# Kernel optimization log

Hardware: AMD Instinct MI355X
Metric: run time of the kernel (lower is better)

Reference implementation:

```python
import jax, jax.numpy as jnp
import numpy as np

B, C, H, W = 1, 256, 48, 64
HW = H * W
HIDDEN, CTX = 128, 64
LEVELS, RADIUS = 4, 4
WIN = 2 * RADIUS + 1
P = WIN * WIN                     # 81 lookup points per level
CORR_DIM = P * LEVELS             # 324
TOP_K = 3
ITERS = 4
STEP_ROT, STEP_TRANS = 0.02, 0.02


def _sample_templates():
    # 12 directions x 3 scales + identity = 37 pose perturbations (as in __init__)
    base = [([0,0,0],[1,0,0]),([0,0,0],[-1,0,0]),([0,0,0],[0,1,0]),([0,0,0],[0,-1,0]),
            ([0,0,0],[0,0,1]),([0,0,0],[0,0,-1]),([1,0,0],[0,0,0]),([-1,0,0],[0,0,0]),
            ([0,1,0],[0,0,0]),([0,-1,0],[0,0,0]),([0,0,1],[0,0,0]),([0,0,-1],[0,0,0])]
    scales = np.array([0.25, 1.0, 4.0], np.float32)
    rot = np.repeat(np.array([r for r, _ in base], np.float32), 3, axis=0)
    trs = np.repeat(np.array([t for _, t in base], np.float32), 3, axis=0)
    sc = np.tile(scales, 12)
    axes = rot / np.clip(np.linalg.norm(rot, axis=1, keepdims=True), 1e-8, None)
    ha = STEP_ROT * sc / 2.0
    dq = np.stack([np.cos(ha), axes[:, 0]*np.sin(ha), axes[:, 1]*np.sin(ha), axes[:, 2]*np.sin(ha)], -1)
    dt = trs * (STEP_TRANS * sc[:, None])
    dq = np.concatenate([dq, [[1., 0., 0., 0.]]], 0)
    dt = np.concatenate([dt, [[0., 0., 0.]]], 0)
    return jnp.asarray(dq), jnp.asarray(dt)

DQ, DT = _sample_templates()     # (37,4), (37,3)
N_SAMPLES = DQ.shape[0]


def qmul(q, r):
    w1, x1, y1, z1 = jnp.moveaxis(q, -1, 0)
    w2, x2, y2, z2 = jnp.moveaxis(r, -1, 0)
    return jnp.stack([w1*w2 - x1*x2 - y1*y2 - z1*z2,
                      w1*x2 + x1*w2 + y1*z2 - z1*y2,
                      w1*y2 - x1*z2 + y1*w2 + z1*x2,
                      w1*z2 + x1*y2 - y1*x2 + z1*w2], -1)


def qapply(q, v):
    qv = jnp.concatenate([jnp.zeros(v.shape[:-1] + (1,), v.dtype), v], -1)
    qc = q * jnp.array([1., -1., -1., -1.], q.dtype)
    return qmul(qmul(q, qv), qc)[..., 1:]


def quat_to_R(q):
    w, x, y, z = jnp.moveaxis(q, -1, 0)
    R = jnp.stack([1-2*(y*y+z*z), 2*(x*y-w*z), 2*(x*z+w*y),
                   2*(x*y+w*z), 1-2*(x*x+z*z), 2*(y*z-w*x),
                   2*(x*z-w*y), 2*(y*z+w*x), 1-2*(x*x+y*y)], -1)
    return R.reshape(q.shape[:-1] + (3, 3))


def conv3(x, w, b):
    y = jax.lax.conv_general_dilated(x, w, (1, 1), 'SAME',
                                     dimension_numbers=('NCHW', 'OIHW', 'NCHW'))
    return y + b[None, :, None, None]


def bilinear_lookup(corr_flat, Hl, Wl, x, y):
    # corr_flat: (B,HW,Hl*Wl); x,y: (B,N,HW,P) -> (B,N,HW,P), zero padding outside
    x0 = jnp.floor(x)
    y0 = jnp.floor(y)
    out = jnp.zeros(x.shape, corr_flat.dtype)
    def gather(idx):
        g = lambda ix: jnp.take_along_axis(corr_flat, ix, axis=-1)
        return jax.vmap(g, in_axes=1, out_axes=1)(idx)   # vmap over N, no corr copy
    for dx_, dy_ in ((0, 0), (1, 0), (0, 1), (1, 1)):
        xi = x0 + dx_
        yi = y0 + dy_
        wgt = (1 - jnp.abs(x - xi)) * (1 - jnp.abs(y - yi))
        valid = (xi >= 0) & (xi < Wl) & (yi >= 0) & (yi < Hl)
        idx = (jnp.clip(yi, 0, Hl - 1) * Wl + jnp.clip(xi, 0, Wl - 1)).astype(jnp.int32)
        out = out + jnp.where(valid, wgt, 0.0) * gather(idx)
    return out


def _forward(fmap_rgb, fmap_depth, depth, context, intrinsics,
             Wz, bz, Wr, br, Wq, bq, Wh, bh, Wfc, bfc):
    f32 = jnp.float32
    fx = 60. + 40. * intrinsics[:, 0]
    fy = 60. + 40. * intrinsics[:, 1]
    cx = W / 2. + 4. * (intrinsics[:, 2] - 0.5)
    cy = H / 2. + 4. * (intrinsics[:, 3] - 0.5)
    d = 4.0 + 20.0 * depth                                  # (B,H,W) metric depth

    # 4D correlation pyramid: corr[b,i,:,:] = <fmap_depth pixel i, fmap_rgb>
    fd = fmap_depth.reshape(B, C, HW).transpose(0, 2, 1)    # (B,HW,C)
    corr = jnp.einsum('bic,bchw->bihw', fd, fmap_rgb) / jnp.sqrt(f32(C))
    pyramid = []
    cl, Hl, Wl = corr, H, W
    for _ in range(LEVELS):
        pyramid.append((cl.reshape(B, HW, Hl * Wl), Hl, Wl))
        cl = cl.reshape(B, HW, Hl // 2, 2, Wl // 2, 2).mean(axis=(3, 5))
        Hl //= 2
        Wl //= 2

    # back-projected depth points (B,HW,3)
    vv, uu = jnp.meshgrid(jnp.arange(H, dtype=f32), jnp.arange(W, dtype=f32), indexing='ij')
    uu = uu.reshape(HW)
    vv = vv.reshape(HW)
    df = d.reshape(B, HW)
    X = jnp.stack([(uu[None] - cx[:, None]) / fx[:, None] * df,
                   (vv[None] - cy[:, None]) / fy[:, None] * df, df], -1)

    off = jnp.arange(-RADIUS, RADIUS + 1, dtype=f32)
    oy, ox = jnp.meshgrid(off, off, indexing='ij')
    ox = ox.reshape(P)
    oy = oy.reshape(P)

    pose = jnp.tile(jnp.array([1., 0., 0., 0., 0., 0., 0.], f32)[None, :], (B, 1))
    h = jnp.zeros((B, HIDDEN, H, W), f32)

    for _ in range(ITERS):
        qc, tc = pose[:, :4], pose[:, 4:7]
        quats = qmul(qc[:, None, :], DQ[None])              # (B,N,4)
        quats = quats / jnp.linalg.norm(quats, axis=-1, keepdims=True)
        trans = tc[:, None, :] + qapply(qc[:, None, :], DT[None])
        Rm = quat_to_R(quats)                               # (B,N,3,3)
        Xc = jnp.einsum('bnij,bpj->bnpi', Rm, X) + trans[:, :, None, :]
        z = jnp.clip(Xc[..., 2], 0.1, None)
        u = fx[:, None, None] * Xc[..., 0] / z + cx[:, None, None]   # (B,N,HW)
        v = fy[:, None, None] * Xc[..., 1] / z + cy[:, None, None]
        feats = []
        for lvl, (cfl, Hl_, Wl_) in enumerate(pyramid):
            s = f32(2 ** lvl)
            xl = u[..., None] / s + ox
            yl = v[..., None] / s + oy
            feats.append(bilinear_lookup(cfl, Hl_, Wl_, xl, yl))
        cf = jnp.concatenate(feats, -1)                     # (B,N,HW,CORR_DIM)
        conf = cf.mean(axis=(2, 3))                         # (B,N) sample confidence
        topv, topi = jax.lax.top_k(conf, TOP_K)
        wk = jax.nn.softmax(topv, axis=-1)                  # confidence-weighted top-K
        idx = jnp.broadcast_to(topi[:, :, None, None], (B, TOP_K, HW, CORR_DIM))
        sel = jnp.take_along_axis(cf, idx, axis=1)
        fused = (wk[:, :, None, None] * sel).sum(1)         # (B,HW,CORR_DIM)
        fused = fused.transpose(0, 2, 1).reshape(B, CORR_DIM, H, W)

        # ConvGRU update
        x_in = jnp.concatenate([fused, context], 1)
        hx = jnp.concatenate([h, x_in], 1)
        zg = jax.nn.sigmoid(conv3(hx, Wz, bz))
        rg = jax.nn.sigmoid(conv3(hx, Wr, br))
        qg = jnp.tanh(conv3(jnp.concatenate([rg * h, x_in], 1), Wq, bq))
        h = (1 - zg) * h + zg * qg

        # 7D pose delta head + quaternion/Lie-style update
        feat = jax.nn.relu(conv3(h, Wh, bh)).mean(axis=(2, 3))
        delta = 0.01 * (feat @ Wfc + bfc)                   # (B,7)
        dq = jnp.concatenate([1.0 + delta[:, :1], delta[:, 1:4]], -1)
        dq = dq / jnp.linalg.norm(dq, axis=-1, keepdims=True)
        tn = tc + qapply(qc, delta[:, 4:7])
        qn = qmul(qc, dq)
        qn = qn / jnp.linalg.norm(qn, axis=-1, keepdims=True)
        pose = jnp.concatenate([qn, tn], -1)
    return pose


def setup_inputs() -> dict:
    key = jax.random.key(0)
    ks = jax.random.split(key, 12)
    rn = lambda k, shape, s=1.0: s * jax.random.normal(k, shape, jnp.float32)
    Gin = HIDDEN + CORR_DIM + CTX
    sc = 1.0 / np.sqrt(Gin * 9)
    sh = 1.0 / np.sqrt(HIDDEN * 9)
    return {
        'fmap_rgb': rn(ks[0], (B, C, H, W)),
        'fmap_depth': rn(ks[1], (B, C, H, W)),
        'depth': jax.random.uniform(ks[2], (B, H, W), jnp.float32),
        'context': rn(ks[3], (B, CTX, H, W)),
        'intrinsics': jax.random.uniform(ks[4], (B, 4), jnp.float32),
        'Wz': rn(ks[5], (HIDDEN, Gin, 3, 3), sc), 'bz': jnp.zeros((HIDDEN,), jnp.float32),
        'Wr': rn(ks[6], (HIDDEN, Gin, 3, 3), sc), 'br': jnp.zeros((HIDDEN,), jnp.float32),
        'Wq': rn(ks[7], (HIDDEN, Gin, 3, 3), sc), 'bq': jnp.zeros((HIDDEN,), jnp.float32),
        'Wh': rn(ks[8], (HIDDEN, HIDDEN, 3, 3), sh), 'bh': jnp.zeros((HIDDEN,), jnp.float32),
        'Wfc': rn(ks[9], (HIDDEN, 7), 1.0 / np.sqrt(HIDDEN)), 'bfc': jnp.zeros((7,), jnp.float32),
    }


def reference(fmap_rgb, fmap_depth, depth, context, intrinsics,
              Wz, bz, Wr, br, Wq, bq, Wh, bh, Wfc, bfc):
    return _forward(fmap_rgb, fmap_depth, depth, context, intrinsics,
                    Wz, bz, Wr, br, Wq, bq, Wh, bh, Wfc, bfc)
```

## Files before the change

kernel.cpp:

```cpp
#include <hip/hip_runtime.h>
#include <math.h>

constexpr int kH = 48, kW = 64, kHW = 3072, kC = 256;
constexpr int kHidden = 128, kCtx = 64;
constexpr int kP = 81, kCorrDim = 324;
constexpr int kNS = 37, kIters = 4;
constexpr int kGin = kHidden + kCorrDim + kCtx;
constexpr int kWp2 = 66, kHp2 = 50, kPix = 3300;
constexpr int kCF = 416;
constexpr int kCHh = 128;

constexpr int kSB0 = 0, kSB1 = 4292, kSB2 = 5720, kSB3 = 6292, kSBTot = 6580;
constexpr int kHB0 = 0, kHB1 = 3552, kHB2 = 4560, kHB3 = 4872, kHBTot = 4980;

constexpr size_t U_CORR0 = 0;
constexpr size_t U_CORR1 = U_CORR0 + (size_t)kHW * 3072;
constexpr size_t U_CORR2 = U_CORR1 + (size_t)kHW * 768;
constexpr size_t U_CORR3 = U_CORR2 + (size_t)kHW * 192;
constexpr size_t U_END0  = U_CORR3 + (size_t)kHW * 48;
constexpr size_t F_X     = U_END0 / 2;
constexpr size_t F_H     = F_X + (size_t)kHW * 3;
constexpr size_t F_ZPRE  = F_H + (size_t)kHidden * kHW;
constexpr size_t F_END1  = F_ZPRE + (size_t)kHidden * kHW;
constexpr size_t U_FCT   = F_END1 * 2;
constexpr size_t U_HT    = U_FCT + (size_t)kPix * kCF;
constexpr size_t U_RHT   = U_HT + (size_t)kPix * kCHh;
constexpr size_t U_PZR   = U_RHT + (size_t)kPix * kCHh;
constexpr size_t U_PQ    = U_PZR + (size_t)16 * 9 * 17 * 512;
constexpr size_t U_PH    = U_PQ + (size_t)8 * 9 * 17 * 512;
constexpr size_t U_END2  = U_PH + (size_t)8 * 9 * 4 * 512;
constexpr size_t F_BZR   = U_END2 / 2 + 1;
constexpr size_t F_CONF  = F_BZR + 256;
constexpr size_t F_POSE  = F_CONF + 64;
constexpr size_t F_FEAT  = F_POSE + 16;
constexpr size_t F_SAMP  = F_FEAT + 128;
constexpr size_t F_END3  = F_SAMP + 448;
constexpr size_t U_FDT   = F_END3 * 2;
constexpr size_t U_QT    = U_FDT + (size_t)kHW * kC;
constexpr size_t U_SBOX  = U_FDT;

typedef __attribute__((ext_vector_type(8))) short short8;
typedef __attribute__((ext_vector_type(4))) float f32x4;

__device__ inline unsigned short f2b(float f) {
  unsigned int u = __float_as_uint(f);
  unsigned int r = u + 0x7FFF + ((u >> 16) & 1);
  return (unsigned short)(r >> 16);
}
__device__ inline float b2f(unsigned short u) {
  return __uint_as_float(((unsigned int)u) << 16);
}
__device__ inline int clampi(int v, int lo, int hi) { return min(max(v, lo), hi); }

__constant__ float c_rot[12][3] = {
  {0,0,0},{0,0,0},{0,0,0},{0,0,0},{0,0,0},{0,0,0},
  {1,0,0},{-1,0,0},{0,1,0},{0,-1,0},{0,0,1},{0,0,-1}};
__constant__ float c_trs[12][3] = {
  {1,0,0},{-1,0,0},{0,1,0},{0,-1,0},{0,0,1},{0,0,-1},
  {0,0,0},{0,0,0},{0,0,0},{0,0,0},{0,0,0},{0,0,0}};

__device__ inline void d_qmul(const float* q, const float* r, float* o) {
  o[0] = q[0]*r[0] - q[1]*r[1] - q[2]*r[2] - q[3]*r[3];
  o[1] = q[0]*r[1] + q[1]*r[0] + q[2]*r[3] - q[3]*r[2];
  o[2] = q[0]*r[2] - q[1]*r[3] + q[2]*r[0] + q[3]*r[1];
  o[3] = q[0]*r[3] + q[1]*r[2] - q[2]*r[1] + q[3]*r[0];
}
__device__ inline void d_qapply(const float* q, const float* v, float* o) {
  float a0 = -q[1]*v[0] - q[2]*v[1] - q[3]*v[2];
  float a1 =  q[0]*v[0] + q[2]*v[2] - q[3]*v[1];
  float a2 =  q[0]*v[1] - q[1]*v[2] + q[3]*v[0];
  float a3 =  q[0]*v[2] + q[1]*v[1] - q[2]*v[0];
  o[0] = -a0*q[1] + a1*q[0] - a2*q[3] + a3*q[2];
  o[1] = -a0*q[2] + a1*q[3] + a2*q[0] - a3*q[1];
  o[2] = -a0*q[3] - a1*q[2] + a2*q[1] + a3*q[0];
}
__device__ inline void d_intr(const float* intr, float& fx, float& fy, float& cx, float& cy) {
  fx = 60.f + 40.f*intr[0];
  fy = 60.f + 40.f*intr[1];
  cx = 32.f + 4.f*(intr[2] - 0.5f);
  cy = 24.f + 4.f*(intr[3] - 0.5f);
}
__device__ inline void sample_Rt(int t, const float* __restrict__ pose, float* S) {
  float qc[4] = {pose[0], pose[1], pose[2], pose[3]};
  float tc[3] = {pose[4], pose[5], pose[6]};
  float dq[4], dt[3];
  if (t == 36) {
    dq[0] = 1.f; dq[1] = dq[2] = dq[3] = 0.f;
    dt[0] = dt[1] = dt[2] = 0.f;
  } else {
    int j = t / 3, k = t % 3;
    float sc = (k == 0) ? 0.25f : ((k == 1) ? 1.f : 4.f);
    float rx = c_rot[j][0], ry = c_rot[j][1], rz = c_rot[j][2];
    float nrm = sqrtf(rx*rx + ry*ry + rz*rz);
    float axn = fmaxf(nrm, 1e-8f);
    float ax = rx / axn, ay = ry / axn, az = rz / axn;
    float ha = 0.02f * sc * 0.5f;
    float sh = sinf(ha), ch = cosf(ha);
    dq[0] = ch; dq[1] = ax * sh; dq[2] = ay * sh; dq[3] = az * sh;
    dt[0] = c_trs[j][0] * (0.02f * sc);
    dt[1] = c_trs[j][1] * (0.02f * sc);
    dt[2] = c_trs[j][2] * (0.02f * sc);
  }
  float qn[4];
  d_qmul(qc, dq, qn);
  float inv = 1.f / sqrtf(qn[0]*qn[0] + qn[1]*qn[1] + qn[2]*qn[2] + qn[3]*qn[3]);
  qn[0] *= inv; qn[1] *= inv; qn[2] *= inv; qn[3] *= inv;
  float tr[3];
  d_qapply(qc, dt, tr);
  float w = qn[0], x = qn[1], y = qn[2], z = qn[3];
  S[0] = 1.f - 2.f*(y*y + z*z); S[1] = 2.f*(x*y - w*z);       S[2] = 2.f*(x*z + w*y);
  S[3] = 2.f*(x*y + w*z);       S[4] = 1.f - 2.f*(x*x + z*z); S[5] = 2.f*(y*z - w*x);
  S[6] = 2.f*(x*z - w*y);       S[7] = 2.f*(y*z + w*x);       S[8] = 1.f - 2.f*(x*x + y*y);
  S[9]  = tc[0] + tr[0];
  S[10] = tc[1] + tr[1];
  S[11] = tc[2] + tr[2];
}
__device__ inline void project_uv(const float* S, const float* Xp, const float* intr,
                                  float& u, float& v) {
  float xc0 = S[0]*Xp[0] + S[1]*Xp[1] + S[2]*Xp[2] + S[9];
  float xc1 = S[3]*Xp[0] + S[4]*Xp[1] + S[5]*Xp[2] + S[10];
  float xc2 = S[6]*Xp[0] + S[7]*Xp[1] + S[8]*Xp[2] + S[11];
  float z = fmaxf(xc2, 0.1f);
  float fx, fy, cx, cy;
  d_intr(intr, fx, fy, cx, cy);
  u = fx * xc0 / z + cx;
  v = fy * xc1 / z + cy;
}

__global__ void init_k(const float* __restrict__ ctx, const float* __restrict__ bz,
                       const float* __restrict__ br, const float* __restrict__ depth,
                       const float* __restrict__ intr, float* __restrict__ h,
                       unsigned int* __restrict__ zbase, unsigned short* __restrict__ fcT,
                       float* __restrict__ bzr, float* __restrict__ X,
                       float* __restrict__ conf, float* __restrict__ feat,
                       float* __restrict__ pose, float* __restrict__ samp) {
  const size_t nz = ((size_t)kPix * (kCF + 2 * kCHh)) / 2;
  for (size_t i = blockIdx.x * blockDim.x + threadIdx.x; i < nz;
       i += (size_t)gridDim.x * blockDim.x)
    zbase[i] = 0;
  int idx = blockIdx.x * blockDim.x + threadIdx.x;
  if (idx < kHidden * kHW) h[idx] = 0.f;
  if (idx < kHW) {
    float fx, fy, cx, cy;
    d_intr(intr, fx, fy, cx, cy);
    float d = 4.f + 20.f * depth[idx];
    float u = (float)(idx % kW), v = (float)(idx / kW);
    X[idx*3+0] = (u - cx) / fx * d;
    X[idx*3+1] = (v - cy) / fy * d;
    X[idx*3+2] = d;
  }
  if (idx < 256) bzr[idx] = (idx < 128) ? bz[idx] : br[idx - 128];
  if (idx < 64) conf[idx] = 0.f;
  if (idx < 128) feat[idx] = 0.f;
  if (idx < kNS) {
    const float ipose[7] = {1.f, 0.f, 0.f, 0.f, 0.f, 0.f, 0.f};
    sample_Rt(idx, ipose, samp + idx * 12);
  }
  if (idx == 0) {
    pose[0] = 1.f;
    for (int j = 1; j < 7; ++j) pose[j] = 0.f;
  }
}
__global__ void initctx_k(const float* __restrict__ ctx, unsigned short* __restrict__ fcT) {
  int idx = blockIdx.x * blockDim.x + threadIdx.x;
  if (idx < kHW * 64) {
    int p = idx >> 6, c = idx & 63;
    int ppix = ((p >> 6) + 1) * kWp2 + (p & 63) + 1;
    fcT[(size_t)ppix * kCF + kCorrDim + c] = f2b(ctx[(size_t)c * kHW + p]);
  }
}

__global__ void pack_k(const float* __restrict__ W0, const float* __restrict__ W1,
                       int ocSplit, int OC, int NCH, int Cin,
                       unsigned short* __restrict__ P) {
  int idx = blockIdx.x * blockDim.x + threadIdx.x;
  int total = (OC / 16) * 9 * NCH * 64;
  if (idx >= total) return;
  int g = idx & 3;
  int m = (idx >> 2) & 15;
  int rest = idx >> 6;
  int cc = rest % NCH;
  int rest2 = rest / NCH;
  int tap = rest2 % 9;
  int ot = rest2 / 9;
  int oc = ot * 16 + m;
  union { unsigned short u[8]; uint4 q; } v;
#pragma unroll
  for (int j = 0; j < 8; ++j) {
    int ci = cc * 32 + g * 8 + j;
    float w = 0.f;
    if (ci < Cin)
      w = (oc < ocSplit) ? W0[((size_t)oc * Cin + ci) * 9 + tap]
                         : W1[((size_t)(oc - ocSplit) * Cin + ci) * 9 + tap];
    v.u[j] = f2b(w);
  }
  *(uint4*)&P[(size_t)idx * 8] = v.q;
}

__global__ __launch_bounds__(256) void t_bf16_k(const float* __restrict__ src,
                                                unsigned short* __restrict__ dst) {
  __shared__ float t[64][65];
  const int tid = threadIdx.x;
  const int p0 = blockIdx.x * 64, c0 = blockIdx.y * 64;
  const int tx = tid & 63, ty = tid >> 6;
  for (int cl = ty; cl < 64; cl += 4)
    t[cl][tx] = src[(size_t)(c0 + cl) * kHW + p0 + tx];
  __syncthreads();
  for (int pl = ty; pl < 64; pl += 4)
    dst[(size_t)(p0 + pl) * kC + c0 + tx] = f2b(t[tx][pl]);
}

__global__ __launch_bounds__(256) void corr_mfma_k(const unsigned short* __restrict__ fdT,
                                                   const unsigned short* __restrict__ qT,
                                                   unsigned short* __restrict__ Cg) {
  const int tid = threadIdx.x;
  const int wv = tid >> 6, lane = tid & 63;
  const int m = lane & 15, kg = lane >> 4;
  const int i0 = blockIdx.y * 128 + wv * 32;
  const int q0 = blockIdx.x * 128;

  f32x4 acc[2][8];
#pragma unroll
  for (int t = 0; t < 2; ++t)
#pragma unroll
    for (int u = 0; u < 8; ++u) acc[t][u] = (f32x4){0.f, 0.f, 0.f, 0.f};

#pragma unroll
  for (int kc = 0; kc < 8; ++kc) {
    const int kb = kc * 32 + kg * 8;
    short8 a[2], b[8];
#pragma unroll
    for (int t = 0; t < 2; ++t)
      a[t] = *(const short8*)&fdT[(size_t)(i0 + t * 16 + m) * kC + kb];
#pragma unroll
    for (int u = 0; u < 8; ++u)
      b[u] = *(const short8*)&qT[(size_t)(q0 + u * 16 + m) * kC + kb];
#pragma unroll
    for (int t = 0; t < 2; ++t)
#pragma unroll
      for (int u = 0; u < 8; ++u)
        acc[t][u] = __builtin_amdgcn_mfma_f32_16x16x32_bf16(a[t], b[u], acc[t][u], 0, 0, 0);
  }
  const float S = 0.0625f;
#pragma unroll
  for (int t = 0; t < 2; ++t)
#pragma unroll
    for (int u = 0; u < 8; ++u)
#pragma unroll
      for (int r = 0; r < 4; ++r)
        Cg[(size_t)(i0 + t * 16 + kg * 4 + r) * kHW + q0 + u * 16 + m] = f2b(acc[t][u][r] * S);
}

template<int HL>
__device__ inline void colpref(float* base, int Wp) {
  float v[HL];
#pragma unroll
  for (int y = 0; y < HL; ++y) v[y] = base[(size_t)y * Wp];
  float run = 0.f;
#pragma unroll
  for (int y = 0; y < HL; ++y) {
    run += v[y];
    base[(size_t)y * Wp] = run;
  }
}

__global__ __launch_bounds__(256) void boxbuild_k(const unsigned short* __restrict__ corr0,
                                                  unsigned short* __restrict__ corr1,
                                                  unsigned short* __restrict__ corr2,
                                                  unsigned short* __restrict__ corr3,
                                                  unsigned short* __restrict__ Sbox) {
  __shared__ float pyr[4080];
  __shared__ float hb[kHBTot];
  const int i = blockIdx.x;
  const int tid = threadIdx.x;
  const int wv = tid >> 6, lane = tid & 63;

  for (int idx = tid; idx < 3072; idx += 256)
    pyr[idx] = b2f(corr0[(size_t)i * 3072 + idx]);
  __syncthreads();

  for (int c = tid; c < 768; c += 256) {
    int y = c >> 5, x = c & 31;
    float v = 0.25f * (pyr[(2*y)*64 + 2*x] + pyr[(2*y)*64 + 2*x + 1] +
                       pyr[(2*y+1)*64 + 2*x] + pyr[(2*y+1)*64 + 2*x + 1]);
    unsigned short b = f2b(v);
    corr1[(size_t)i * 768 + c] = b;
    pyr[3072 + c] = b2f(b);
  }
  __syncthreads();
  for (int c = tid; c < 192; c += 256) {
    int y = c >> 4, x = c & 15;
    const float* p = pyr + 3072;
    float v = 0.25f * (p[(2*y)*32 + 2*x] + p[(2*y)*32 + 2*x + 1] +
                       p[(2*y+1)*32 + 2*x] + p[(2*y+1)*32 + 2*x + 1]);
    unsigned short b = f2b(v);
    corr2[(size_t)i * 192 + c] = b;
    pyr[3840 + c] = b2f(b);
  }
  __syncthreads();
  for (int c = tid; c < 48; c += 256) {
    int y = c >> 3, x = c & 7;
    const float* p = pyr + 3840;
    float v = 0.25f * (p[(2*y)*16 + 2*x] + p[(2*y)*16 + 2*x + 1] +
                       p[(2*y+1)*16 + 2*x] + p[(2*y+1)*16 + 2*x + 1]);
    unsigned short b = f2b(v);
    corr3[(size_t)i * 48 + c] = b;
    pyr[4032 + c] = b2f(b);
  }
  __syncthreads();

  const int lvl_off[4] = {0, 3072, 3840, 4032};
  for (int r = wv; r < 90; r += 4) {
    int lvl, y;
    if (r < 48)      { lvl = 0; y = r; }
    else if (r < 72) { lvl = 1; y = r - 48; }
    else if (r < 84) { lvl = 2; y = r - 72; }
    else             { lvl = 3; y = r - 84; }
    const int Wl = kW >> lvl;
    float* row = &pyr[lvl_off[lvl] + y * Wl];
    float v = (lane < Wl) ? row[lane] : 0.f;
#pragma unroll
    for (int o = 1; o < 64; o <<= 1) {
      float tv = __shfl_up(v, o, 64);
      if (lane >= o) v += tv;
    }
    if (lane < Wl) row[lane] = v;
  }
  __syncthreads();

  for (int c = tid; c < 3552; c += 256) {
    int y = c / 74, as = c % 74;
    const float* pref = &pyr[y * 64];
    float Hv = 0.f;
    if (as >= 1) Hv = pref[min(63, as - 1)];
    if (as >= 10) Hv -= pref[as - 10];
    hb[kHB0 + c] = Hv;
  }
  for (int c = tid; c < 1008; c += 256) {
    int y = c / 42, as = c % 42;
    const float* pref = &pyr[3072 + y * 32];
    float Hv = 0.f;
    if (as >= 1) Hv = pref[min(31, as - 1)];
    if (as >= 10) Hv -= pref[as - 10];
    hb[kHB1 + c] = Hv;
  }
  for (int c = tid; c < 312; c += 256) {
    int y = c / 26, as = c % 26;
    const float* pref = &pyr[3840 + y * 16];
    float Hv = 0.f;
    if (as >= 1) Hv = pref[min(15, as - 1)];
    if (as >= 10) Hv -= pref[as - 10];
    hb[kHB2 + c] = Hv;
  }
  for (int c = tid; c < 108; c += 256) {
    int y = c / 18, as = c % 18;
    const float* pref = &pyr[4032 + y * 8];
    float Hv = 0.f;
    if (as >= 1) Hv = pref[min(7, as - 1)];
    if (as >= 10) Hv -= pref[as - 10];
    hb[kHB3 + c] = Hv;
  }
  __syncthreads();

  if (tid < 160) {
    if (tid < 74)       colpref<48>(hb + kHB0 + tid, 74);
    else if (tid < 116) colpref<24>(hb + kHB1 + (tid - 74), 42);
    else if (tid < 142) colpref<12>(hb + kHB2 + (tid - 116), 26);
    else                colpref<6>(hb + kHB3 + (tid - 142), 18);
  }
  __syncthreads();

  unsigned short* out = Sbox + (size_t)i * kSBTot;
  for (int c = tid; c < 4292; c += 256) {
    int bp = c / 74, as = c % 74;
    const float* col = &hb[kHB0 + as];
    float S = 0.f;
    if (bp >= 1) S = col[min(47, bp - 1) * 74];
    if (bp >= 10) S -= col[(bp - 10) * 74];
    out[kSB0 + c] = f2b(S);
  }
  for (int c = tid; c < 1428; c += 256) {
    int bp = c / 42, as = c % 42;
    const float* col = &hb[kHB1 + as];
    float S = 0.f;
    if (bp >= 1) S = col[min(23, bp - 1) * 42];
    if (bp >= 10) S -= col[(bp - 10) * 42];
    out[kSB1 + c] = f2b(S);
  }
  for (int c = tid; c < 572; c += 256) {
    int bp = c / 26, as = c % 26;
    const float* col = &hb[kHB2 + as];
    float S = 0.f;
    if (bp >= 1) S = col[min(11, bp - 1) * 26];
    if (bp >= 10) S -= col[(bp - 10) * 26];
    out[kSB2 + c] = f2b(S);
  }
  for (int c = tid; c < 288; c += 256) {
    int bp = c / 18, as = c % 18;
    const float* col = &hb[kHB3 + as];
    float S = 0.f;
    if (bp >= 1) S = col[min(5, bp - 1) * 18];
    if (bp >= 10) S -= col[(bp - 10) * 18];
    out[kSB3 + c] = f2b(S);
  }
}

__global__ __launch_bounds__(256) void conf_k(const unsigned short* __restrict__ Sbox,
                                              const float* __restrict__ X,
                                              const float* __restrict__ samp,
                                              const float* __restrict__ intr,
                                              float* __restrict__ conf) {
  const int idx = blockIdx.x * 256 + threadIdx.x;
  const int n = idx / kHW, i = idx - n * kHW;
  const float* S = samp + n * 12;
  float Xp[3] = {X[i*3], X[i*3+1], X[i*3+2]};
  float u, v;
  project_uv(S, Xp, intr, u, v);
  const unsigned short* sb = Sbox + (size_t)i * kSBTot;
  float tot = 0.f;
#pragma unroll
  for (int l = 0; l < 4; ++l) {
    const int Wp = (kW >> l) + 10, Hp = (kH >> l) + 10;
    const int so = (l == 0) ? kSB0 : (l == 1) ? kSB1 : (l == 2) ? kSB2 : kSB3;
    const float s = (float)(1 << l);
    const float bx = u / s, by = v / s;
    const float fbx = floorf(bx), fby = floorf(by);
    const int x0 = (int)fbx, y0 = (int)fby;
    const float fx = bx - fbx, fy = by - fby;
    const int xa = clampi(x0 + 5, 0, Wp - 1), xb = clampi(x0 + 6, 0, Wp - 1);
    const int ya = clampi(y0 + 5, 0, Hp - 1), yb = clampi(y0 + 6, 0, Hp - 1);
    const float s00 = b2f(sb[so + ya * Wp + xa]), s10 = b2f(sb[so + ya * Wp + xb]);
    const float s01 = b2f(sb[so + yb * Wp + xa]), s11 = b2f(sb[so + yb * Wp + xb]);
    tot += (1.f - fx) * (1.f - fy) * s00 + fx * (1.f - fy) * s10 +
           (1.f - fx) * fy * s01 + fx * fy * s11;
  }
#pragma unroll
  for (int o = 32; o; o >>= 1) tot += __shfl_xor(tot, o, 64);
  if ((threadIdx.x & 63) == 0) atomicAdd(&conf[n], tot);
}

__global__ __launch_bounds__(256) void fused_k(const unsigned short* __restrict__ corr0,
                                               const unsigned short* __restrict__ corr1,
                                               const unsigned short* __restrict__ corr2,
                                               const unsigned short* __restrict__ corr3,
                                               const float* __restrict__ X,
                                               const float* __restrict__ samp,
                                               const float* __restrict__ intr,
                                               const float* __restrict__ conf,
                                               unsigned short* __restrict__ fcT) {
  __shared__ float win[12][10][12];
  __shared__ float s_fx[12], s_fy[12];
  __shared__ int   s_ix[12], s_iy[12];
  __shared__ float s_w[3];
  __shared__ int   s_id[3];
  const int i = blockIdx.x;
  const int tid = threadIdx.x;

  if (tid == 0) {
    const float scale = 1.f / ((float)kHW * (float)kCorrDim);
    float c[kNS];
    for (int n = 0; n < kNS; ++n) c[n] = conf[n] * scale;
    int id[3] = {-1, -1, -1};
    float v[3];
    for (int k = 0; k < 3; ++k) {
      float best = -1e30f;
      int bi = -1;
      for (int n = 0; n < kNS; ++n) {
        if (n == id[0] || n == id[1] || n == id[2]) continue;
        if (c[n] > best) { best = c[n]; bi = n; }
      }
      v[k] = best;
      id[k] = bi;
    }
    float m = v[0];
    float e0 = expf(v[0] - m), e1 = expf(v[1] - m), e2 = expf(v[2] - m);
    float s = e0 + e1 + e2;
    s_w[0] = e0 / s; s_w[1] = e1 / s; s_w[2] = e2 / s;
    s_id[0] = id[0]; s_id[1] = id[1]; s_id[2] = id[2];
  }
  __syncthreads();

  if (tid < 3) {
    const float* S = samp + s_id[tid] * 12;
    float Xp[3] = {X[i*3], X[i*3+1], X[i*3+2]};
    float u, v;
    project_uv(S, Xp, intr, u, v);
#pragma unroll
    for (int l = 0; l < 4; ++l) {
      float s = (float)(1 << l);
      float bx = u / s, by = v / s;
      float fbx = floorf(bx), fby = floorf(by);
      s_ix[tid*4 + l] = (int)fbx;
      s_iy[tid*4 + l] = (int)fby;
      s_fx[tid*4 + l] = bx - fbx;
      s_fy[tid*4 + l] = by - fby;
    }
  }
  __syncthreads();

  for (int sidx = tid; sidx < 1200; sidx += 256) {
    const int w = sidx / 100, rem = sidx % 100;
    const int rr = rem / 10, cc = rem % 10;
    const int lvl = w & 3;
    const int Wl = kW >> lvl, Hl = kH >> lvl;
    const unsigned short* base =
        (lvl == 0) ? corr0 : (lvl == 1) ? corr1 : (lvl == 2) ? corr2 : corr3;
    const int y = s_iy[w] - 4 + rr;
    const int x = s_ix[w] - 4 + cc;
    float v = 0.f;
    if (y >= 0 && y < Hl && x >= 0 && x < Wl)
      v = b2f(base[(size_t)i * (Hl * Wl) + y * Wl + x]);
    win[w][rr][cc] = v;
  }
  __syncthreads();

  const int ppix = ((i >> 6) + 1) * kWp2 + (i & 63) + 1;
  for (int d = tid; d < kCorrDim; d += 256) {
    const int lvl = d / kP;
    const int o = d % kP;
    const int oyi = o / 9, oxi = o % 9;
    float val = 0.f;
#pragma unroll
    for (int k = 0; k < 3; ++k) {
      const int w = k * 4 + lvl;
      const float fx = s_fx[w], fy = s_fy[w];
      const float w00 = (1.f - fx) * (1.f - fy), w10 = fx * (1.f - fy);
      const float w01 = (1.f - fx) * fy, w11 = fx * fy;
      val += s_w[k] * (w00 * win[w][oyi][oxi] + w10 * win[w][oyi][oxi + 1] +
                       w01 * win[w][oyi + 1][oxi] + w11 * win[w][oyi + 1][oxi + 1]);
    }
    fcT[(size_t)ppix * kCF + d] = f2b(val);
  }
}

template<int CCB, int CCE, int NCHH, int NCHTOT>
__device__ inline void conv_core32(const unsigned short* __restrict__ srcH,
                                   const unsigned short* __restrict__ srcF,
                                   const unsigned short* __restrict__ A,
                                   int y, int xbase, int ot, int lane,
                                   f32x4 (&acc)[2]) {
  const int m = lane & 15, kg = lane >> 4;
  const unsigned short* a_base = A + (size_t)ot * (9 * NCHTOT * 512) + m * 32 + kg * 8;
  const int pix0 = (y + 1) * kWp2 + (xbase + 1) + m;
#pragma unroll
  for (int tap = 0; tap < 9; ++tap) {
    const int dy = tap / 3 - 1, dx = tap % 3 - 1;
    const int po = pix0 + dy * kWp2 + dx;
    const unsigned short* bh0 = srcH + (size_t)po * kCHh + kg * 8;
    const unsigned short* bf0 = srcF + (size_t)po * kCF + kg * 8;
#pragma unroll
    for (int cc = CCB; cc < CCE; ++cc) {
      const int s = tap * NCHTOT + cc;
      short8 a = *(const short8*)(a_base + (size_t)s * 512);
      short8 b0, b1;
      if (cc < NCHH) {
        b0 = *(const short8*)(bh0 + cc * 32);
        b1 = *(const short8*)(bh0 + 16 * kCHh + cc * 32);
      } else {
        b0 = *(const short8*)(bf0 + (cc - NCHH) * 32);
        b1 = *(const short8*)(bf0 + 16 * kCF + (cc - NCHH) * 32);
      }
      acc[0] = __builtin_amdgcn_mfma_f32_16x16x32_bf16(a, b0, acc[0], 0, 0, 0);
      acc[1] = __builtin_amdgcn_mfma_f32_16x16x32_bf16(a, b1, acc[1], 0, 0, 0);
    }
  }
}

__global__ __launch_bounds__(256) void conv_zr_k(const unsigned short* __restrict__ hT,
                                                 const unsigned short* __restrict__ fcT,
                                                 const unsigned short* __restrict__ P,
                                                 const float* __restrict__ bzr,
                                                 float* __restrict__ zpre,
                                                 const float* __restrict__ hbuf,
                                                 unsigned short* __restrict__ rhT) {
  __shared__ f32x4 red[3][2][64];
  const int tid = threadIdx.x;
  const int wv = tid >> 6, lane = tid & 63;
  const int y = blockIdx.y >> 1, xbase = (blockIdx.y & 1) * 32;
  const int ot = blockIdx.x;
  f32x4 acc[2] = {{0.f,0.f,0.f,0.f},{0.f,0.f,0.f,0.f}};
  if (wv == 0)      conv_core32<0, 5, 4, 17>(hT, fcT, P, y, xbase, ot, lane, acc);
  else if (wv == 1) conv_core32<5, 9, 4, 17>(hT, fcT, P, y, xbase, ot, lane, acc);
  else if (wv == 2) conv_core32<9, 13, 4, 17>(hT, fcT, P, y, xbase, ot, lane, acc);
  else              conv_core32<13, 17, 4, 17>(hT, fcT, P, y, xbase, ot, lane, acc);
  if (wv != 0) {
    red[wv - 1][0][lane] = acc[0];
    red[wv - 1][1][lane] = acc[1];
  }
  __syncthreads();
  if (wv != 0) return;
#pragma unroll
  for (int j = 0; j < 3; ++j) {
    acc[0] += red[j][0][lane];
    acc[1] += red[j][1][lane];
  }
  const int m = lane & 15, kg = lane >> 4;
#pragma unroll
  for (int t = 0; t < 2; ++t)
#pragma unroll
    for (int r = 0; r < 4; ++r) {
      const int oc = ot * 16 + kg * 4 + r;
      const int pxx = xbase + t * 16 + m;
      const int px = y * kW + pxx;
      const float val = acc[t][r] + bzr[oc];
      if (oc < kHidden) {
        zpre[(size_t)oc * kHW + px] = val;
      } else {
        const float rg = 1.f / (1.f + expf(-val));
        const int ppix = (y + 1) * kWp2 + pxx + 1;
        rhT[(size_t)ppix * kCHh + oc - kHidden] =
            f2b(rg * hbuf[(size_t)(oc - kHidden) * kHW + px]);
      }
    }
}

__global__ __launch_bounds__(256) void conv_q_k(const unsigned short* __restrict__ rhT,
                                                const unsigned short* __restrict__ fcT,
                                                unsigned short* __restrict__ hT,
                                                const unsigned short* __restrict__ P,
                                                const float* __restrict__ bq,
                                                const float* __restrict__ zpre,
                                                float* __restrict__ hbuf) {
  __shared__ f32x4 red[3][2][64];
  const int tid = threadIdx.x;
  const int wv = tid >> 6, lane = tid & 63;
  const int y = blockIdx.y >> 1, xbase = (blockIdx.y & 1) * 32;
  const int ot = blockIdx.x;
  f32x4 acc[2] = {{0.f,0.f,0.f,0.f},{0.f,0.f,0.f,0.f}};
  if (wv == 0)      conv_core32<0, 5, 4, 17>(rhT, fcT, P, y, xbase, ot, lane, acc);
  else if (wv == 1) conv_core32<5, 9, 4, 17>(rhT, fcT, P, y, xbase, ot, lane, acc);
  else if (wv == 2) conv_core32<9, 13, 4, 17>(rhT, fcT, P, y, xbase, ot, lane, acc);
  else              conv_core32<13, 17, 4, 17>(rhT, fcT, P, y, xbase, ot, lane, acc);
  if (wv != 0) {
    red[wv - 1][0][lane] = acc[0];
    red[wv - 1][1][lane] = acc[1];
  }
  __syncthreads();
  if (wv != 0) return;
#pragma unroll
  for (int j = 0; j < 3; ++j) {
    acc[0] += red[j][0][lane];
    acc[1] += red[j][1][lane];
  }
  const int m = lane & 15, kg = lane >> 4;
#pragma unroll
  for (int t = 0; t < 2; ++t)
#pragma unroll
    for (int r = 0; r < 4; ++r) {
      const int oc = ot * 16 + kg * 4 + r;
      const int pxx = xbase + t * 16 + m;
      const int px = y * kW + pxx;
      const size_t off = (size_t)oc * kHW + px;
      const float q = acc[t][r] + bq[oc];
      const float zg = 1.f / (1.f + expf(-zpre[off]));
      const float hn = (1.f - zg) * hbuf[off] + zg * tanhf(q);
      hbuf[off] = hn;
      const int ppix = (y + 1) * kWp2 + pxx + 1;
      hT[(size_t)ppix * kCHh + oc] = f2b(hn);
    }
}

__global__ __launch_bounds__(256) void conv_h_k(const unsigned short* __restrict__ hT,
                                                const unsigned short* __restrict__ P,
                                                const float* __restrict__ bh,
                                                float* __restrict__ feat) {
  __shared__ f32x4 red[2][2][64];
  const int tid = threadIdx.x;
  const int wv = tid >> 6, lane = tid & 63;
  const int p = wv >> 1, half = wv & 1;
  const int y = blockIdx.y >> 1, xbase = (blockIdx.y & 1) * 32;
  const int ot = blockIdx.x * 2 + p;
  f32x4 acc[2] = {{0.f,0.f,0.f,0.f},{0.f,0.f,0.f,0.f}};
  if (half == 0) conv_core32<0, 2, 4, 4>(hT, hT, P, y, xbase, ot, lane, acc);
  else           conv_core32<2, 4, 4, 4>(hT, hT, P, y, xbase, ot, lane, acc);
  if (half == 1) {
    red[p][0][lane] = acc[0];
    red[p][1][lane] = acc[1];
  }
  __syncthreads();
  if (half != 0) return;
  acc[0] += red[p][0][lane];
  acc[1] += red[p][1][lane];
  const int m = lane & 15, kg = lane >> 4;
#pragma unroll
  for (int r = 0; r < 4; ++r) {
    const int oc = ot * 16 + kg * 4 + r;
    const float bv = bh[oc];
    float v = fmaxf(acc[0][r] + bv, 0.f) + fmaxf(acc[1][r] + bv, 0.f);
    v += __shfl_xor(v, 1, 64);
    v += __shfl_xor(v, 2, 64);
    v += __shfl_xor(v, 4, 64);
    v += __shfl_xor(v, 8, 64);
    if (m == 0) atomicAdd(&feat[oc], v);
  }
}

__global__ void pose_update_k(float* __restrict__ feat, float* __restrict__ conf,
                              const float* __restrict__ Wfc,
                              const float* __restrict__ bfc, float* __restrict__ pose,
                              float* __restrict__ samp, float* __restrict__ out) {
  __shared__ float s_d[7];
  __shared__ float s_pose[7];
  int t = threadIdx.x;
  if (t < 7) {
    float s = 0.f;
    const float inv = 1.f / (float)kHW;
    for (int k = 0; k < kHidden; ++k) s += (feat[k] * inv) * Wfc[k * 7 + t];
    s_d[t] = 0.01f * (s + bfc[t]);
  }
  __syncthreads();
  if (t < kHidden) feat[t] = 0.f;
  if (t < 64) conf[t] = 0.f;
  if (t == 0) {
    float qc[4] = {pose[0], pose[1], pose[2], pose[3]};
    float tc[3] = {pose[4], pose[5], pose[6]};
    float dq[4] = {1.f + s_d[0], s_d[1], s_d[2], s_d[3]};
    float inv = 1.f / sqrtf(dq[0]*dq[0] + dq[1]*dq[1] + dq[2]*dq[2] + dq[3]*dq[3]);
    dq[0] *= inv; dq[1] *= inv; dq[2] *= inv; dq[3] *= inv;
    float dv[3] = {s_d[4], s_d[5], s_d[6]};
    float rv[3];
    d_qapply(qc, dv, rv);
    float tn[3] = {tc[0] + rv[0], tc[1] + rv[1], tc[2] + rv[2]};
    float qn[4];
    d_qmul(qc, dq, qn);
    float inv2 = 1.f / sqrtf(qn[0]*qn[0] + qn[1]*qn[1] + qn[2]*qn[2] + qn[3]*qn[3]);
    qn[0] *= inv2; qn[1] *= inv2; qn[2] *= inv2; qn[3] *= inv2;
    s_pose[0] = qn[0]; s_pose[1] = qn[1]; s_pose[2] = qn[2]; s_pose[3] = qn[3];
    s_pose[4] = tn[0]; s_pose[5] = tn[1]; s_pose[6] = tn[2];
    pose[0] = qn[0]; pose[1] = qn[1]; pose[2] = qn[2]; pose[3] = qn[3];
    pose[4] = tn[0]; pose[5] = tn[1]; pose[6] = tn[2];
    out[0] = qn[0]; out[1] = qn[1]; out[2] = qn[2]; out[3] = qn[3];
    out[4] = tn[0]; out[5] = tn[1]; out[6] = tn[2];
  }
  __syncthreads();
  if (t < kNS) sample_Rt(t, s_pose, samp + t * 12);
}

extern "C" void kernel_launch(void* const* d_in, const int* in_sizes, int n_in,
                              void* d_out, int out_size, void* d_ws, size_t ws_size,
                              hipStream_t stream) {
  const float* frgb  = (const float*)d_in[0];
  const float* fdep  = (const float*)d_in[1];
  const float* depth = (const float*)d_in[2];
  const float* ctx   = (const float*)d_in[3];
  const float* intr  = (const float*)d_in[4];
  const float* Wz = (const float*)d_in[5];
  const float* bz = (const float*)d_in[6];
  const float* Wr = (const float*)d_in[7];
  const float* br = (const float*)d_in[8];
  const float* Wq = (const float*)d_in[9];
  const float* bq = (const float*)d_in[10];
  const float* Wh = (const float*)d_in[11];
  const float* bh = (const float*)d_in[12];
  const float* Wfc = (const float*)d_in[13];
  const float* bfc = (const float*)d_in[14];
  float* outp = (float*)d_out;

  float* ws = (float*)d_ws;
  unsigned short* us = (unsigned short*)d_ws;
  unsigned short* corr0 = us + U_CORR0;
  unsigned short* corr1 = us + U_CORR1;
  unsigned short* corr2 = us + U_CORR2;
  unsigned short* corr3 = us + U_CORR3;
  float* X    = ws + F_X;
  float* hbuf = ws + F_H;
  float* zpre = ws + F_ZPRE;
  unsigned short* fcT = us + U_FCT;
  unsigned short* hT  = us + U_HT;
  unsigned short* rhT = us + U_RHT;
  unsigned short* Pzr = us + U_PZR;
  unsigned short* Pq  = us + U_PQ;
  unsigned short* Ph  = us + U_PH;
  float* bzr  = ws + F_BZR;
  float* conf = ws + F_CONF;
  float* pose = ws + F_POSE;
  float* feat = ws + F_FEAT;
  float* samp = ws + F_SAMP;
  unsigned short* fdT  = us + U_FDT;
  unsigned short* qT   = us + U_QT;
  unsigned short* Sbox = us + U_SBOX;

  init_k<<<1536, 256, 0, stream>>>(ctx, bz, br, depth, intr, hbuf,
                                   (unsigned int*)fcT, fcT, bzr, X, conf, feat,
                                   pose, samp);
  initctx_k<<<768, 256, 0, stream>>>(ctx, fcT);
  pack_k<<<(16 * 9 * 17 * 64 + 255) / 256, 256, 0, stream>>>(Wz, Wr, 128, 256, 17,
                                                             kGin, Pzr);
  pack_k<<<(8 * 9 * 17 * 64 + 255) / 256, 256, 0, stream>>>(Wq, Wq, 128, 128, 17,
                                                            kGin, Pq);
  pack_k<<<(8 * 9 * 4 * 64 + 255) / 256, 256, 0, stream>>>(Wh, Wh, 128, 128, 4,
                                                           kHidden, Ph);
  t_bf16_k<<<dim3(48, 4), 256, 0, stream>>>(fdep, fdT);
  t_bf16_k<<<dim3(48, 4), 256, 0, stream>>>(frgb, qT);
  corr_mfma_k<<<dim3(24, 24), 256, 0, stream>>>(fdT, qT, corr0);
  boxbuild_k<<<kHW, 256, 0, stream>>>(corr0, corr1, corr2, corr3, Sbox);

  for (int it = 0; it < kIters; ++it) {
    conf_k<<<444, 256, 0, stream>>>(Sbox, X, samp, intr, conf);
    fused_k<<<kHW, 256, 0, stream>>>(corr0, corr1, corr2, corr3, X, samp, intr,
                                     conf, fcT);
    conv_zr_k<<<dim3(16, 96), 256, 0, stream>>>(hT, fcT, Pzr, bzr, zpre, hbuf, rhT);
    conv_q_k<<<dim3(8, 96), 256, 0, stream>>>(rhT, fcT, hT, Pq, bq, zpre, hbuf);
    conv_h_k<<<dim3(4, 96), 256, 0, stream>>>(hT, Ph, bh, feat);
    pose_update_k<<<1, 128, 0, stream>>>(feat, conf, Wfc, bfc, pose, samp, outp);
  }
}
```

Before: 775.8 us.

## Merge setup kernels and fold pose update into conv_h via last-block counter

Combines the context transpose and three weight-pack launches into one setup kernel, and merges the two fp32-to-bf16 transposes into a single grid. The per-iteration pose_update kernel is folded into conv_h_k: each block bumps a global counter after its feat atomics, and the last of the 384 blocks runs the pose update and resets the counter. This removes several launches and the launch gaps between them, at the cost of a threadfence and atomic per block and reliance on correct last-block ordering.

```diff
diff --git a/kernel.cpp b/kernel.cpp
--- a/kernel.cpp
+++ b/kernel.cpp
@@ -34,7 +34,8 @@
 constexpr size_t F_POSE  = F_CONF + 64;
 constexpr size_t F_FEAT  = F_POSE + 16;
 constexpr size_t F_SAMP  = F_FEAT + 128;
-constexpr size_t F_END3  = F_SAMP + 448;
+constexpr size_t F_CNT   = F_SAMP + 448;
+constexpr size_t F_END3  = F_CNT + 16;
 constexpr size_t U_FDT   = F_END3 * 2;
 constexpr size_t U_QT    = U_FDT + (size_t)kHW * kC;
 constexpr size_t U_SBOX  = U_FDT;
@@ -133,7 +134,8 @@
                        unsigned int* __restrict__ zbase, unsigned short* __restrict__ fcT,
                        float* __restrict__ bzr, float* __restrict__ X,
                        float* __restrict__ conf, float* __restrict__ feat,
-                       float* __restrict__ pose, float* __restrict__ samp) {
+                       float* __restrict__ pose, float* __restrict__ samp,
+                       unsigned int* __restrict__ cnt) {
   const size_t nz = ((size_t)kPix * (kCF + 2 * kCHh)) / 2;
   for (size_t i = blockIdx.x * blockDim.x + threadIdx.x; i < nz;
        i += (size_t)gridDim.x * blockDim.x)
@@ -159,23 +161,13 @@
   if (idx == 0) {
     pose[0] = 1.f;
     for (int j = 1; j < 7; ++j) pose[j] = 0.f;
-  }
-}
-__global__ void initctx_k(const float* __restrict__ ctx, unsigned short* __restrict__ fcT) {
-  int idx = blockIdx.x * blockDim.x + threadIdx.x;
-  if (idx < kHW * 64) {
-    int p = idx >> 6, c = idx & 63;
-    int ppix = ((p >> 6) + 1) * kWp2 + (p & 63) + 1;
-    fcT[(size_t)ppix * kCF + kCorrDim + c] = f2b(ctx[(size_t)c * kHW + p]);
-  }
-}
-
-__global__ void pack_k(const float* __restrict__ W0, const float* __restrict__ W1,
-                       int ocSplit, int OC, int NCH, int Cin,
-                       unsigned short* __restrict__ P) {
-  int idx = blockIdx.x * blockDim.x + threadIdx.x;
-  int total = (OC / 16) * 9 * NCH * 64;
-  if (idx >= total) return;
+    *cnt = 0;
+  }
+}
+
+__device__ inline void pack_one(const float* __restrict__ W0, const float* __restrict__ W1,
+                                int ocSplit, int NCH, int Cin,
+                                unsigned short* __restrict__ P, int idx) {
   int g = idx & 3;
   int m = (idx >> 2) & 15;
   int rest = idx >> 6;
@@ -197,11 +189,35 @@
   *(uint4*)&P[(size_t)idx * 8] = v.q;
 }
 
-__global__ __launch_bounds__(256) void t_bf16_k(const float* __restrict__ src,
-                                                unsigned short* __restrict__ dst) {
+__global__ void setup2_k(const float* __restrict__ ctx, unsigned short* __restrict__ fcT,
+                         const float* __restrict__ Wz, const float* __restrict__ Wr,
+                         const float* __restrict__ Wq, const float* __restrict__ Wh,
+                         unsigned short* __restrict__ Pzr, unsigned short* __restrict__ Pq,
+                         unsigned short* __restrict__ Ph) {
+  int idx = blockIdx.x * blockDim.x + threadIdx.x;
+  if (idx < 196608) {
+    int p = idx >> 6, c = idx & 63;
+    int ppix = ((p >> 6) + 1) * kWp2 + (p & 63) + 1;
+    fcT[(size_t)ppix * kCF + kCorrDim + c] = f2b(ctx[(size_t)c * kHW + p]);
+  } else if (idx < 353280) {
+    pack_one(Wz, Wr, 128, 17, kGin, Pzr, idx - 196608);
+  } else if (idx < 431616) {
+    pack_one(Wq, Wq, 128, 17, kGin, Pq, idx - 353280);
+  } else if (idx < 450048) {
+    pack_one(Wh, Wh, 128, 4, kHidden, Ph, idx - 431616);
+  }
+}
+
+__global__ __launch_bounds__(256) void t_bf16_k(const float* __restrict__ fdep,
+                                                const float* __restrict__ frgb,
+                                                unsigned short* __restrict__ fdT,
+                                                unsigned short* __restrict__ qT) {
   __shared__ float t[64][65];
   const int tid = threadIdx.x;
-  const int p0 = blockIdx.x * 64, c0 = blockIdx.y * 64;
+  const int which = blockIdx.y >> 2;
+  const float* src = which ? frgb : fdep;
+  unsigned short* dst = which ? qT : fdT;
+  const int p0 = blockIdx.x * 64, c0 = (blockIdx.y & 3) * 64;
   const int tx = tid & 63, ty = tid >> 6;
   for (int cl = ty; cl < 64; cl += 4)
     t[cl][tx] = src[(size_t)(c0 + cl) * kHW + p0 + tx];
@@ -663,8 +679,16 @@
 __global__ __launch_bounds__(256) void conv_h_k(const unsigned short* __restrict__ hT,
                                                 const unsigned short* __restrict__ P,
                                                 const float* __restrict__ bh,
-                                                float* __restrict__ feat) {
+                                                float* __restrict__ feat,
+                                                float* __restrict__ conf,
+                                                const float* __restrict__ Wfc,
+                                                const float* __restrict__ bfc,
+                                                float* __restrict__ pose,
+                                                float* __restrict__ samp,
+                                                float* __restrict__ out,
+                                                unsigned int* __restrict__ cnt) {
   __shared__ f32x4 red[2][2][64];
+  __shared__ unsigned int s_last;
   const int tid = threadIdx.x;
   const int wv = tid >> 6, lane = tid & 63;
   const int p = wv >> 1, half = wv & 1;
@@ -678,40 +702,41 @@
     red[p][1][lane] = acc[1];
   }
   __syncthreads();
-  if (half != 0) return;
-  acc[0] += red[p][0][lane];
-  acc[1] += red[p][1][lane];
-  const int m = lane & 15, kg = lane >> 4;
-#pragma unroll
-  for (int r = 0; r < 4; ++r) {
-    const int oc = ot * 16 + kg * 4 + r;
-    const float bv = bh[oc];
-    float v = fmaxf(acc[0][r] + bv, 0.f) + fmaxf(acc[1][r] + bv, 0.f);
-    v += __shfl_xor(v, 1, 64);
-    v += __shfl_xor(v, 2, 64);
-    v += __shfl_xor(v, 4, 64);
-    v += __shfl_xor(v, 8, 64);
-    if (m == 0) atomicAdd(&feat[oc], v);
-  }
-}
-
-__global__ void pose_update_k(float* __restrict__ feat, float* __restrict__ conf,
-                              const float* __restrict__ Wfc,
-                              const float* __restrict__ bfc, float* __restrict__ pose,
-                              float* __restrict__ samp, float* __restrict__ out) {
+  if (half == 0) {
+    acc[0] += red[p][0][lane];
+    acc[1] += red[p][1][lane];
+    const int m = lane & 15, kg = lane >> 4;
+#pragma unroll
+    for (int r = 0; r < 4; ++r) {
+      const int oc = ot * 16 + kg * 4 + r;
+      const float bv = bh[oc];
+      float v = fmaxf(acc[0][r] + bv, 0.f) + fmaxf(acc[1][r] + bv, 0.f);
+      v += __shfl_xor(v, 1, 64);
+      v += __shfl_xor(v, 2, 64);
+      v += __shfl_xor(v, 4, 64);
+      v += __shfl_xor(v, 8, 64);
+      if (m == 0) atomicAdd(&feat[oc], v);
+    }
+  }
+  __threadfence();
+  __syncthreads();
+  if (tid == 0) s_last = (atomicAdd(cnt, 1u) == 383u) ? 1u : 0u;
+  __syncthreads();
+  if (!s_last) return;
+
   __shared__ float s_d[7];
   __shared__ float s_pose[7];
-  int t = threadIdx.x;
-  if (t < 7) {
+  volatile const float* vfeat = feat;
+  if (tid < 7) {
     float s = 0.f;
     const float inv = 1.f / (float)kHW;
-    for (int k = 0; k < kHidden; ++k) s += (feat[k] * inv) * Wfc[k * 7 + t];
-    s_d[t] = 0.01f * (s + bfc[t]);
-  }
-  __syncthreads();
-  if (t < kHidden) feat[t] = 0.f;
-  if (t < 64) conf[t] = 0.f;
-  if (t == 0) {
+    for (int k = 0; k < kHidden; ++k) s += (vfeat[k] * inv) * Wfc[k * 7 + tid];
+    s_d[tid] = 0.01f * (s + bfc[tid]);
+  }
+  __syncthreads();
+  if (tid < kHidden) feat[tid] = 0.f;
+  if (tid < 64) conf[tid] = 0.f;
+  if (tid == 0) {
     float qc[4] = {pose[0], pose[1], pose[2], pose[3]};
     float tc[3] = {pose[4], pose[5], pose[6]};
     float dq[4] = {1.f + s_d[0], s_d[1], s_d[2], s_d[3]};
@@ -731,9 +756,10 @@
     pose[4] = tn[0]; pose[5] = tn[1]; pose[6] = tn[2];
     out[0] = qn[0]; out[1] = qn[1]; out[2] = qn[2]; out[3] = qn[3];
     out[4] = tn[0]; out[5] = tn[1]; out[6] = tn[2];
-  }
-  __syncthreads();
-  if (t < kNS) sample_Rt(t, s_pose, samp + t * 12);
+    *cnt = 0;
+  }
+  __syncthreads();
+  if (tid < kNS) sample_Rt(tid, s_pose, samp + tid * 12);
 }
 
 extern "C" void kernel_launch(void* const* d_in, const int* in_sizes, int n_in,
@@ -776,22 +802,17 @@
   float* pose = ws + F_POSE;
   float* feat = ws + F_FEAT;
   float* samp = ws + F_SAMP;
+  unsigned int* cnt = (unsigned int*)(ws + F_CNT);
   unsigned short* fdT  = us + U_FDT;
   unsigned short* qT   = us + U_QT;
   unsigned short* Sbox = us + U_SBOX;
 
   init_k<<<1536, 256, 0, stream>>>(ctx, bz, br, depth, intr, hbuf,
                                    (unsigned int*)fcT, fcT, bzr, X, conf, feat,
-                                   pose, samp);
-  initctx_k<<<768, 256, 0, stream>>>(ctx, fcT);
-  pack_k<<<(16 * 9 * 17 * 64 + 255) / 256, 256, 0, stream>>>(Wz, Wr, 128, 256, 17,
-                                                             kGin, Pzr);
-  pack_k<<<(8 * 9 * 17 * 64 + 255) / 256, 256, 0, stream>>>(Wq, Wq, 128, 128, 17,
-                                                            kGin, Pq);
-  pack_k<<<(8 * 9 * 4 * 64 + 255) / 256, 256, 0, stream>>>(Wh, Wh, 128, 128, 4,
-                                                           kHidden, Ph);
-  t_bf16_k<<<dim3(48, 4), 256, 0, stream>>>(fdep, fdT);
-  t_bf16_k<<<dim3(48, 4), 256, 0, stream>>>(frgb, qT);
+                                   pose, samp, cnt);
+  setup2_k<<<(450048 + 255) / 256, 256, 0, stream>>>(ctx, fcT, Wz, Wr, Wq, Wh,
+                                                     Pzr, Pq, Ph);
+  t_bf16_k<<<dim3(48, 8), 256, 0, stream>>>(fdep, frgb, fdT, qT);
   corr_mfma_k<<<dim3(24, 24), 256, 0, stream>>>(fdT, qT, corr0);
   boxbuild_k<<<kHW, 256, 0, stream>>>(corr0, corr1, corr2, corr3, Sbox);
 
@@ -801,7 +822,7 @@
                                      conf, fcT);
     conv_zr_k<<<dim3(16, 96), 256, 0, stream>>>(hT, fcT, Pzr, bzr, zpre, hbuf, rhT);
     conv_q_k<<<dim3(8, 96), 256, 0, stream>>>(rhT, fcT, hT, Pq, bq, zpre, hbuf);
-    conv_h_k<<<dim3(4, 96), 256, 0, stream>>>(hT, Ph, bh, feat);
-    pose_update_k<<<1, 128, 0, stream>>>(feat, conf, Wfc, bfc, pose, samp, outp);
-  }
-}
+    conv_h_k<<<dim3(4, 96), 256, 0, stream>>>(hT, Ph, bh, feat, conf, Wfc, bfc,
+                                              pose, samp, outp, cnt);
+  }
+}
```

New measurement: 859.0 us. 1.11x slower.
